# Optimization experiments

Measured on AMD Instinct MI355X. Metric: run time of the kernel, lower is better.

The kernel has to match this reference:

```python
import jax, jax.numpy as jnp
import numpy as np

THRESHOLD = 0.5   # IoU suppression threshold (init arg)
MAX_OUT = 300     # max kept boxes (init arg)
N = 8192          # number of proposals


def setup_inputs() -> dict:
    key = jax.random.key(0)
    k1, k2, k3 = jax.random.split(key, 3)
    # valid xyxy boxes inside an ~800px image
    xy = jax.random.uniform(k1, (N, 2), minval=0.0, maxval=800.0)
    wh = jax.random.uniform(k2, (N, 2), minval=1.0, maxval=200.0)
    rois = jnp.concatenate([xy, xy + wh], axis=1)  # [N,4]
    scores = jax.random.uniform(k3, (N,))
    return {"rois": rois, "scores": scores}


def _pairwise_iou(b):
    # b: [N,4] xyxy
    area = (b[:, 2] - b[:, 0]) * (b[:, 3] - b[:, 1])          # [N]
    lt = jnp.maximum(b[:, None, :2], b[None, :, :2])           # [N,N,2]
    rb = jnp.minimum(b[:, None, 2:], b[None, :, 2:])           # [N,N,2]
    wh = jnp.clip(rb - lt, 0.0)
    inter = wh[..., 0] * wh[..., 1]                            # [N,N]
    return inter / (area[:, None] + area[None, :] - inter)


def reference(rois, scores):
    # sort boxes by descending score (torchvision nms semantics)
    order = jnp.argsort(-scores)           # [N] original indices, score-sorted
    b = rois[order]
    iou = _pairwise_iou(b)                 # [N,N] in score order
    idx = jnp.arange(N)

    # greedy suppression: iterate in score order; a kept box suppresses all
    # later boxes with IoU > threshold
    def body(i, suppressed):
        kept_i = jnp.logical_not(suppressed[i])
        newly = kept_i & (iou[i] > THRESHOLD) & (idx > i)
        return suppressed | newly

    suppressed = jax.lax.fori_loop(0, N, body, jnp.zeros((N,), jnp.bool_))
    keep_mask = jnp.logical_not(suppressed)

    # gather kept sorted-positions (stable, fixed shape); pad with -1
    pos = jnp.sort(jnp.where(keep_mask, idx, N))[:MAX_OUT]     # [MAX_OUT]
    keep = jnp.where(pos < N, order[jnp.minimum(pos, N - 1)], -1)
    return keep  # [MAX_OUT] int32 original indices, -1 padded
```

## Files before the change

### kernel.cpp

```cpp
#include <hip/hip_runtime.h>
#include <stdint.h>
#include <math.h>

#pragma clang fp contract(off)

#define N        8192
#define NCHUNK   128
#define NTILE    64
#define MAX_OUT  300
#define BLIM     32
#define TLIM     14

__global__ void nms_rank_partial(const float* __restrict__ scores,
                                 int* __restrict__ rank32) {
    __shared__ uint32_t sk[256];
    const int tid = threadIdx.x;
    const int bi  = blockIdx.y, bj = blockIdx.x;
    const int jbase = bj * 256;

    sk[tid] = __float_as_uint(scores[jbase + tid]);
    __syncthreads();

    const int i = bi * 256 + tid;
    const uint32_t my = __float_as_uint(scores[i]);

    int cnt = 0;
    const uint4* sk4 = (const uint4*)sk;
    for (int jj = 0; jj < 64; ++jj) {
        uint4 v = sk4[jj];
        int j0 = jbase + jj * 4;
        cnt += (v.x > my) || (v.x == my && (j0 + 0) < i);
        cnt += (v.y > my) || (v.y == my && (j0 + 1) < i);
        cnt += (v.z > my) || (v.z == my && (j0 + 2) < i);
        cnt += (v.w > my) || (v.w == my && (j0 + 3) < i);
    }
    rank32[bj * N + i] = cnt;
}

__global__ void nms_scatter(const float4* __restrict__ rois,
                            const int*    __restrict__ rank32,
                            float4* __restrict__ sboxes,
                            int*    __restrict__ sidx) {
    const int i = blockIdx.x * blockDim.x + threadIdx.x;
    int r = 0;
#pragma unroll
    for (int k = 0; k < 32; ++k) r += rank32[k * N + i];
    sboxes[r] = rois[i];
    sidx[r]   = i;
}

__device__ __forceinline__ uint64_t iou_word(const float4 cb, const float ac,
                                             const float4* __restrict__ rb,
                                             const float*  __restrict__ ra,
                                             const bool diag, const int lane) {
    uint64_t myword = 0;
    for (int r = 0; r < 64; ++r) {
        const float4 b  = rb[r];
        const float  ar = ra[r];
        float lx    = fmaxf(b.x, cb.x);
        float ly    = fmaxf(b.y, cb.y);
        float hx    = fminf(b.z, cb.z);
        float hy    = fminf(b.w, cb.w);
        float w     = fmaxf(hx - lx, 0.0f);
        float h     = fmaxf(hy - ly, 0.0f);
        float inter = w * h;
        float denom = (ar + ac) - inter;
        double di = (double)inter, dd = (double)denom;
        bool sup = (di + di) > (dd + dd * 0x1p-24);
        uint64_t word = __ballot(sup);
        if (diag)
            word &= (r == 63) ? 0ull : (~0ull << (r + 1));
        myword = (lane == r) ? word : myword;
    }
    return myword;
}

__global__ void __launch_bounds__(64)
nms_mask_pruned(const float4* __restrict__ sboxes,
                uint64_t* __restrict__ maskT) {
    const int L = blockIdx.x;
    int bi = (int)(32.5 - sqrt(1056.25 - 2.0 * (double)L));
    if (bi < 0) bi = 0;
    if (bi > 31) bi = 31;
    while (bi < 31 && (bi + 1) * 32 - ((bi + 1) * bi) / 2 <= L) ++bi;
    while (bi > 0 && bi * 32 - (bi * (bi - 1)) / 2 > L) --bi;
    const int bj = bi + (L - (bi * 32 - (bi * (bi - 1)) / 2));

    const int lane = threadIdx.x;
    const float4 cb = sboxes[bj * 64 + lane];
    const float  ac = (cb.z - cb.x) * (cb.w - cb.y);

    __shared__ float4 rb[64];
    __shared__ float  ra[64];
    {
        float4 t = sboxes[bi * 64 + lane];
        rb[lane] = t;
        ra[lane] = (t.z - t.x) * (t.w - t.y);
    }
    __syncthreads();

    uint64_t myword = iou_word(cb, ac, rb, ra, bi == bj, lane);
    maskT[(size_t)bj * N + bi * 64 + lane] = myword;
}

__global__ void __launch_bounds__(256)
nms_mask_rest(const float4* __restrict__ sboxes,
              uint64_t* __restrict__ maskT,
              const int* __restrict__ flag) {
    if (flag[0] == 0) return;
    const int bi  = blockIdx.y;
    const int bjq = blockIdx.x;
    const int w    = threadIdx.x >> 6;
    const int lane = threadIdx.x & 63;
    const int bj   = bjq * 4 + w;

    __shared__ float4 rb[64];
    __shared__ float  ra[64];
    if (threadIdx.x < 64) {
        float4 t = sboxes[bi * 64 + threadIdx.x];
        rb[threadIdx.x] = t;
        ra[threadIdx.x] = (t.z - t.x) * (t.w - t.y);
    }
    __syncthreads();

    if (bj < bi) return;
    if (bi < BLIM && bj < BLIM) return;

    const float4 cb = sboxes[bj * 64 + lane];
    const float  ac = (cb.z - cb.x) * (cb.w - cb.y);
    uint64_t myword = iou_word(cb, ac, rb, ra, bi == bj, lane);
    maskT[(size_t)bj * N + bi * 64 + lane] = myword;
}

__device__ __forceinline__ uint64_t rl64(uint64_t v, int l) {
    uint32_t lo = (uint32_t)__builtin_amdgcn_readlane((int)(uint32_t)v, l);
    uint32_t hi = (uint32_t)__builtin_amdgcn_readlane((int)(uint32_t)(v >> 32), l);
    return ((uint64_t)hi << 32) | lo;
}

template<bool TRYMODE>
__global__ void __launch_bounds__(1024)
nms_scan_k(const uint64_t* __restrict__ maskT,
           const int*      __restrict__ sidx,
           int*            __restrict__ out,
           int*            __restrict__ flag) {
    __shared__ uint32_t removed32[2 * NCHUNK];
    __shared__ uint64_t pf[2][7][64];
    __shared__ uint64_t s_kmask[NCHUNK];
    __shared__ int      s_kbase[NCHUNK];
    __shared__ int      s_klist[448];
    __shared__ int      s_ksnap[2];
    __shared__ int      s_kept, s_done, s_nch;

    if (!TRYMODE) {
        if (flag[0] == 0) return;
    }

    const int t    = threadIdx.x;
    const int lane = t & 63;
    const int wave = t >> 6;

    if (t < 2 * NCHUNK) removed32[t] = 0;
    if (t == 0) { s_kept = 0; s_done = 0; s_nch = 0; s_ksnap[0] = 0; s_ksnap[1] = 0; }
    if (wave == 1) {
        pf[0][0][lane] = maskT[(size_t)0 * N + 0 * 64 + lane];
        pf[0][1][lane] = maskT[(size_t)1 * N + 1 * 64 + lane];
        pf[0][2][lane] = maskT[(size_t)1 * N + 0 * 64 + lane];
        pf[0][3][lane] = maskT[(size_t)2 * N + 0 * 64 + lane];
        pf[0][4][lane] = maskT[(size_t)2 * N + 1 * 64 + lane];
        pf[0][5][lane] = maskT[(size_t)3 * N + 0 * 64 + lane];
        pf[0][6][lane] = maskT[(size_t)3 * N + 1 * 64 + lane];
    }
    __syncthreads();

    const int TEND = TRYMODE ? TLIM : NTILE;
    for (int it = 0; it < TEND; ++it) {
        const int c0 = 2 * it, c1 = 2 * it + 1;
        const int buf = it & 1;

        if (wave == 0) {
            uint64_t D0  = pf[buf][0][lane], D1  = pf[buf][1][lane];
            uint64_t X   = pf[buf][2][lane];
            uint64_t Y0a = pf[buf][3][lane], Y0b = pf[buf][4][lane];
            uint64_t Y1a = pf[buf][5][lane], Y1b = pf[buf][6][lane];
            uint64_t rem0 = (uint64_t)removed32[2 * c0] | ((uint64_t)removed32[2 * c0 + 1] << 32);
            uint64_t rem1 = (uint64_t)removed32[2 * c1] | ((uint64_t)removed32[2 * c1 + 1] << 32);
            uint64_t keep0 = 0, keep1 = 0, xw = 0, y0 = 0, y1 = 0;

            uint64_t cand = ~rem0;
            while (cand) {
                int l = __builtin_ctzll(cand);
                keep0 |= (1ull << l);
                uint64_t d = rl64(D0, l);
                xw |= rl64(X, l);
                y0 |= rl64(Y0a, l);
                y1 |= rl64(Y1a, l);
                cand &= ~d;
                cand &= ~(1ull << l);
            }
            rem1 |= xw;
            cand = ~rem1;
            while (cand) {
                int l = __builtin_ctzll(cand);
                keep1 |= (1ull << l);
                uint64_t d = rl64(D1, l);
                y0 |= rl64(Y0b, l);
                y1 |= rl64(Y1b, l);
                cand &= ~d;
                cand &= ~(1ull << l);
            }
            if (c0 + 2 < NCHUNK && y0) {
                atomicOr(&removed32[2 * (c0 + 2)],     (uint32_t)y0);
                atomicOr(&removed32[2 * (c0 + 2) + 1], (uint32_t)(y0 >> 32));
            }
            if (c0 + 3 < NCHUNK && y1) {
                atomicOr(&removed32[2 * (c0 + 3)],     (uint32_t)y1);
                atomicOr(&removed32[2 * (c0 + 3) + 1], (uint32_t)(y1 >> 32));
            }
            const int n0 = __popcll(keep0), n1 = __popcll(keep1);
            const int base = s_kept;
            if ((keep0 >> lane) & 1) {
                int p = __popcll(keep0 & ((1ull << lane) - 1ull));
                s_klist[base + p] = c0 * 64 + lane;
            }
            if ((keep1 >> lane) & 1) {
                int p = n0 + __popcll(keep1 & ((1ull << lane) - 1ull));
                s_klist[base + p] = c1 * 64 + lane;
            }
            if (lane == 0) {
                s_kmask[c0] = keep0;  s_kmask[c1] = keep1;
                s_kbase[c0] = base;   s_kbase[c1] = base + n0;
                int nk      = base + n0 + n1;
                s_kept      = nk;
                s_ksnap[(it + 1) & 1] = nk;
                s_nch       = c1 + 1;
                if (TRYMODE) {
                    if (nk >= MAX_OUT) s_done = 1;
                } else {
                    if (nk >= MAX_OUT || it == NTILE - 1) s_done = 1;
                }
            }
        } else if (wave == 1) {
            const int p0 = 2 * it + 2, p1 = 2 * it + 3;
            const int m0 = 2 * it + 4, m1 = 2 * it + 5;
            if (p0 < NCHUNK) {
                pf[buf ^ 1][0][lane] = maskT[(size_t)p0 * N + p0 * 64 + lane];
                pf[buf ^ 1][1][lane] = maskT[(size_t)p1 * N + p1 * 64 + lane];
                pf[buf ^ 1][2][lane] = maskT[(size_t)p1 * N + p0 * 64 + lane];
                if (m0 < NCHUNK) {
                    pf[buf ^ 1][3][lane] = maskT[(size_t)m0 * N + p0 * 64 + lane];
                    pf[buf ^ 1][4][lane] = maskT[(size_t)m0 * N + p1 * 64 + lane];
                    pf[buf ^ 1][5][lane] = maskT[(size_t)m1 * N + p0 * 64 + lane];
                    pf[buf ^ 1][6][lane] = maskT[(size_t)m1 * N + p1 * 64 + lane];
                }
            }
        } else {
            if (it >= 1) {
                const int kprev = s_ksnap[it & 1];
                const int col   = c0 + 2 + (wave & 1);
                const int idx   = ((wave - 2) >> 1) * 64 + lane;
                uint64_t v = 0;
                if (idx < kprev && col < NCHUNK)
                    v = maskT[(size_t)col * N + s_klist[idx]];
                v |= (uint64_t)__shfl_xor((unsigned long long)v, 1);
                v |= (uint64_t)__shfl_xor((unsigned long long)v, 2);
                v |= (uint64_t)__shfl_xor((unsigned long long)v, 4);
                v |= (uint64_t)__shfl_xor((unsigned long long)v, 8);
                v |= (uint64_t)__shfl_xor((unsigned long long)v, 16);
                v |= (uint64_t)__shfl_xor((unsigned long long)v, 32);
                if (lane == 0 && v != 0 && col < NCHUNK) {
                    atomicOr(&removed32[2 * col],     (uint32_t)v);
                    atomicOr(&removed32[2 * col + 1], (uint32_t)(v >> 32));
                }
            }
        }
        __syncthreads();
        if (s_done) break;
    }

    if (TRYMODE) {
        if (t == 0) flag[0] = s_done ? 0 : 1;
        if (!s_done) return;
    }

    const int nch = s_nch;
    for (int cp = t >> 6; cp < nch; cp += 16) {
        uint64_t km = s_kmask[cp];
        if ((km >> lane) & 1) {
            int pos = s_kbase[cp] + __popcll(km & ((1ull << lane) - 1ull));
            if (pos < MAX_OUT) out[pos] = sidx[cp * 64 + lane];
        }
    }
    const int start = s_kept < MAX_OUT ? s_kept : MAX_OUT;
    for (int p = start + t; p < MAX_OUT; p += 1024) out[p] = -1;
}

extern "C" void kernel_launch(void* const* d_in, const int* in_sizes, int n_in,
                              void* d_out, int out_size, void* d_ws, size_t ws_size,
                              hipStream_t stream) {
    const float4* rois   = (const float4*)d_in[0];
    const float*  scores = (const float*)d_in[1];
    int* out = (int*)d_out;

    float4*   sboxes = (float4*)d_ws;
    int*      sidx   = (int*)((char*)d_ws + 128 * 1024);
    uint64_t* maskT  = (uint64_t*)((char*)d_ws + 160 * 1024);
    int*      rank32 = (int*)((char*)d_ws + 160 * 1024 + 8 * 1024 * 1024);
    int*      flag   = (int*)((char*)d_ws + 160 * 1024 + 9 * 1024 * 1024);

    nms_rank_partial<<<dim3(32, 32), dim3(256), 0, stream>>>(scores, rank32);
    nms_scatter<<<dim3(32), dim3(256), 0, stream>>>(rois, rank32, sboxes, sidx);
    nms_mask_pruned<<<dim3(528), dim3(64), 0, stream>>>(sboxes, maskT);
    nms_scan_k<true><<<dim3(1), dim3(1024), 0, stream>>>(maskT, sidx, out, flag);
    nms_mask_rest<<<dim3(32, 128), dim3(256), 0, stream>>>(sboxes, maskT, flag);
    nms_scan_k<false><<<dim3(1), dim3(1024), 0, stream>>>(maskT, sidx, out, flag);
}
```

Before: 101.8 us.

## Replace serial greedy chunk resolution with wave-parallel fixed-point iteration

The per-chunk greedy suppression loop, which walked kept candidates one by one via readlane, is replaced by a fixed-point iteration. Each step ORs the suppression rows of all currently kept lanes with a butterfly shuffle reduction and repeats until the kept mask stabilizes. Cross-chunk contributions are then computed with single wave-wide OR reductions. This aims to shorten the serial dependency chain on the critical wave, at the cost of several shuffle rounds per iteration and a data-dependent iteration count.

```diff
diff --git a/kernel.cpp b/kernel.cpp
--- a/kernel.cpp
+++ b/kernel.cpp
@@ -132,10 +132,28 @@
     maskT[(size_t)bj * N + bi * 64 + lane] = myword;
 }
 
-__device__ __forceinline__ uint64_t rl64(uint64_t v, int l) {
-    uint32_t lo = (uint32_t)__builtin_amdgcn_readlane((int)(uint32_t)v, l);
-    uint32_t hi = (uint32_t)__builtin_amdgcn_readlane((int)(uint32_t)(v >> 32), l);
+__device__ __forceinline__ uint64_t shflx64(uint64_t v, int m) {
+    uint32_t lo = (uint32_t)__shfl_xor((unsigned int)(v & 0xffffffffull), m, 64);
+    uint32_t hi = (uint32_t)__shfl_xor((unsigned int)(v >> 32), m, 64);
     return ((uint64_t)hi << 32) | lo;
+}
+__device__ __forceinline__ uint64_t wave_or64(uint64_t v) {
+#pragma unroll
+    for (int m = 1; m < 64; m <<= 1) v |= shflx64(v, m);
+    return v;
+}
+
+__device__ __forceinline__ uint64_t resolve_chunk(uint64_t D, uint64_t cand,
+                                                  int lane) {
+    uint64_t kept = cand;
+    for (int itr = 0; itr < 66; ++itr) {
+        uint64_t contrib = ((kept >> lane) & 1) ? D : 0ull;
+        uint64_t S = wave_or64(contrib);
+        uint64_t nk = cand & ~S;
+        if (nk == kept) break;
+        kept = nk;
+    }
+    return kept;
 }
 
 template<bool TRYMODE>
@@ -185,30 +203,19 @@
             uint64_t Y1a = pf[buf][5][lane], Y1b = pf[buf][6][lane];
             uint64_t rem0 = (uint64_t)removed32[2 * c0] | ((uint64_t)removed32[2 * c0 + 1] << 32);
             uint64_t rem1 = (uint64_t)removed32[2 * c1] | ((uint64_t)removed32[2 * c1 + 1] << 32);
-            uint64_t keep0 = 0, keep1 = 0, xw = 0, y0 = 0, y1 = 0;
-
-            uint64_t cand = ~rem0;
-            while (cand) {
-                int l = __builtin_ctzll(cand);
-                keep0 |= (1ull << l);
-                uint64_t d = rl64(D0, l);
-                xw |= rl64(X, l);
-                y0 |= rl64(Y0a, l);
-                y1 |= rl64(Y1a, l);
-                cand &= ~d;
-                cand &= ~(1ull << l);
-            }
+
+            uint64_t keep0 = resolve_chunk(D0, ~rem0, lane);
+            uint64_t m0 = ((keep0 >> lane) & 1) ? ~0ull : 0ull;
+            uint64_t xw = wave_or64(X   & m0);
+            uint64_t y0 = wave_or64(Y0a & m0);
+            uint64_t y1 = wave_or64(Y1a & m0);
+
             rem1 |= xw;
-            cand = ~rem1;
-            while (cand) {
-                int l = __builtin_ctzll(cand);
-                keep1 |= (1ull << l);
-                uint64_t d = rl64(D1, l);
-                y0 |= rl64(Y0b, l);
-                y1 |= rl64(Y1b, l);
-                cand &= ~d;
-                cand &= ~(1ull << l);
-            }
+            uint64_t keep1 = resolve_chunk(D1, ~rem1, lane);
+            uint64_t m1 = ((keep1 >> lane) & 1) ? ~0ull : 0ull;
+            y0 |= wave_or64(Y0b & m1);
+            y1 |= wave_or64(Y1b & m1);
+
             if (c0 + 2 < NCHUNK && y0) {
                 atomicOr(&removed32[2 * (c0 + 2)],     (uint32_t)y0);
                 atomicOr(&removed32[2 * (c0 + 2) + 1], (uint32_t)(y0 >> 32));
@@ -262,12 +269,7 @@
                 uint64_t v = 0;
                 if (idx < kprev && col < NCHUNK)
                     v = maskT[(size_t)col * N + s_klist[idx]];
-                v |= (uint64_t)__shfl_xor((unsigned long long)v, 1);
-                v |= (uint64_t)__shfl_xor((unsigned long long)v, 2);
-                v |= (uint64_t)__shfl_xor((unsigned long long)v, 4);
-                v |= (uint64_t)__shfl_xor((unsigned long long)v, 8);
-                v |= (uint64_t)__shfl_xor((unsigned long long)v, 16);
-                v |= (uint64_t)__shfl_xor((unsigned long long)v, 32);
+                v = wave_or64(v);
                 if (lane == 0 && v != 0 && col < NCHUNK) {
                     atomicOr(&removed32[2 * col],     (uint32_t)v);
                     atomicOr(&removed32[2 * col + 1], (uint32_t)(v >> 32));
```

Measured after the change: 108.9 us. 7.0% more time.
